# Kernel optimization log

Hardware: AMD Instinct MI355X
Metric: run time of the kernel (lower is better)

Reference implementation:

```python
import jax, jax.numpy as jnp
import numpy as np

# static sizes
B = 32          # graphs
NPER = 1024     # nodes per graph
N0 = B * NPER
F_IN = 128
H = 4           # heads
DH = 32         # per-head dim (128/4)
HID = H * DH    # 128
E = 524288      # edges (avg degree 16)
K1, K2, K3 = 512, 256, 128  # ceil(0.5*nper) per stage
NC = 10


def gcn_agg(h, src, dst, w, n):
    """GCNConv propagation: sym-normalized aggregation with self-loops.
    h: [n,F] already projected; w: [E] edge weight (0 for filtered edges)."""
    deg = jax.ops.segment_sum(w, dst, num_segments=n) + 1.0  # +1 self-loop
    dinv = jax.lax.rsqrt(deg)
    coef = dinv[src] * dinv[dst] * w                          # [E]
    agg = jax.ops.segment_sum(h[src] * coef[:, None], dst, num_segments=n)
    return agg + h / deg[:, None]  # self-loop term: dinv[i]^2 = 1/deg[i]


def mh_gcn(x, W, b, src, dst, w, n):
    """MAGPoolGCNLayer: per-head GCNConv (32->32), relu, concat heads."""
    h = jnp.einsum('nhd,hde->nhe', x.reshape(n, H, DH), W).reshape(n, HID)
    return jax.nn.relu(gcn_agg(h, src, dst, w, n) + b.reshape(HID))


def att_pool(x, src, dst, w, A, psW, psb, n, k):
    """MultiHeadAtt: standard att, complex score, concat pooling, global weight."""
    sub = x.reshape(n, H, DH)
    att = jnp.einsum('nhd,hd->nh', sub, A)            # per-head Linear(32,1)
    cat = (att[:, :, None] * sub).reshape(n, HID)     # score*sub, concat
    score = (gcn_agg(cat @ psW, src, dst, w, n) + psb)[:, 0]  # GCNConv(HID,1)
    nper = n // B
    _, idx = jax.lax.top_k(score.reshape(B, nper), k)  # per-graph topk
    perm = (idx + jnp.arange(B)[:, None] * nper).reshape(-1)
    xn = x[perm] * jnp.tanh(score[perm])[:, None]      # global att weighting
    # filter_adj: remap kept nodes, mask edges touching dropped nodes
    nmap = jnp.full((n,), -1, jnp.int32).at[perm].set(jnp.arange(B * k, dtype=jnp.int32))
    ns, nd = nmap[src], nmap[dst]
    wn = w * ((ns >= 0) & (nd >= 0)).astype(w.dtype)
    return xn, jnp.maximum(ns, 0), jnp.maximum(nd, 0), wn


def readout(x):
    # graphs are contiguous with equal node counts -> reshape readout
    xr = x.reshape(B, -1, x.shape[-1])
    return jnp.concatenate([xr.max(1), xr.mean(1)], axis=1)  # [B, 2*HID]


def setup_inputs():
    key = jax.random.key(0)
    ks = jax.random.split(key, 26)
    gid = jnp.repeat(jnp.arange(B, dtype=jnp.int32), E // B)
    src = jax.random.randint(ks[0], (E,), 0, NPER, dtype=jnp.int32) + gid * NPER
    dst = jax.random.randint(ks[1], (E,), 0, NPER, dtype=jnp.int32) + gid * NPER
    x = jax.random.normal(ks[2], (N0, F_IN), jnp.float32)
    s = 0.1
    def rn(k, shp):
        return jax.random.normal(k, shp, jnp.float32) * s
    return {
        'x': x, 'src': src, 'dst': dst,
        'W1': rn(ks[3], (H, DH, DH)), 'b1': rn(ks[4], (H, DH)), 'A1': rn(ks[5], (H, DH)),
        'ps1W': rn(ks[6], (HID, 1)), 'ps1b': rn(ks[7], (1,)),
        'W2': rn(ks[8], (H, DH, DH)), 'b2': rn(ks[9], (H, DH)), 'A2': rn(ks[10], (H, DH)),
        'ps2W': rn(ks[11], (HID, 1)), 'ps2b': rn(ks[12], (1,)),
        'W3': rn(ks[13], (H, DH, DH)), 'b3': rn(ks[14], (H, DH)), 'A3': rn(ks[15], (H, DH)),
        'ps3W': rn(ks[16], (HID, 1)), 'ps3b': rn(ks[17], (1,)),
        'l1W': rn(ks[18], (2 * HID, HID)), 'l1b': rn(ks[19], (HID,)),
        'l2W': rn(ks[20], (HID, HID // 2)), 'l2b': rn(ks[21], (HID // 2,)),
        'l3W': rn(ks[22], (HID // 2, NC)), 'l3b': rn(ks[23], (NC,)),
    }


def reference(x, src, dst, W1, b1, A1, ps1W, ps1b, W2, b2, A2, ps2W, ps2b,
              W3, b3, A3, ps3W, ps3b, l1W, l1b, l2W, l2b, l3W, l3b):
    w = jnp.ones((E,), x.dtype)
    h = mh_gcn(x, W1, b1, src, dst, w, N0)
    h, s1, d1, w1 = att_pool(h, src, dst, w, A1, ps1W, ps1b, N0, K1)
    r1 = readout(h)
    n1 = B * K1
    h = mh_gcn(h, W2, b2, s1, d1, w1, n1)
    h, s2, d2, w2 = att_pool(h, s1, d1, w1, A2, ps2W, ps2b, n1, K2)
    r2 = readout(h)
    n2 = B * K2
    h = mh_gcn(h, W3, b3, s2, d2, w2, n2)
    h, _, _, _ = att_pool(h, s2, d2, w2, A3, ps3W, ps3b, n2, K3)
    r3 = readout(h)
    z = r1 + r2 + r3                      # [B, 2*HID]
    z = jax.nn.relu(z @ l1W + l1b)        # dropout skipped (eval mode)
    z = jax.nn.relu(z @ l2W + l2b)
    return jax.nn.log_softmax(z @ l3W + l3b, axis=-1)
```

## Files before the change

kernel.cpp:

```cpp
#include <hip/hip_runtime.h>
#include <math.h>

#define BGR 32
#define NPER0 1024
#define N0 (BGR * NPER0)
#define FDIM 128
#define EDG 524288
#define EPG (EDG / BGR)
#define EBLK (EDG / 256)
#define K1 512
#define K2 256
#define K3 128
#define N1 (BGR * K1)
#define N2 (BGR * K2)
#define CAP 64
#define RSEC (BGR * FDIM)

__device__ __forceinline__ unsigned enc_f(float v) {
    unsigned u = __float_as_uint(v);
    return (u & 0x80000000u) ? ~u : (u | 0x80000000u);
}
__device__ __forceinline__ float dec_f(unsigned u) {
    return (u & 0x80000000u) ? __uint_as_float(u ^ 0x80000000u) : __uint_as_float(~u);
}

__global__ void bin_kernel(const int* __restrict__ src, const int* __restrict__ dst,
                           int* __restrict__ cnt, int* __restrict__ slot,
                           unsigned* __restrict__ rmax, float* __restrict__ rsum) {
    if (blockIdx.x < BGR) {
        int z = blockIdx.x * 256 + threadIdx.x;
        rmax[z] = 0u;
        rsum[z] = 0.0f;
    }
    const int g = blockIdx.x & 31, chunk = blockIdx.x >> 5;
    int e = g * EPG + chunk * 256 + threadIdx.x;
    int s = src[e];
    int d = dst[e];
    int p = atomicAdd(&cnt[d], 1);
    if (p < CAP) slot[(size_t)d * CAP + p] = s;
}

__global__ void aggw_kernel(const float* __restrict__ xsrc,
                            const int* __restrict__ permIn,
                            const float* __restrict__ multIn,
                            const int* __restrict__ cnt, const int* __restrict__ slot,
                            const float* __restrict__ W, const float* __restrict__ b,
                            const float* __restrict__ A, const float* __restrict__ psW,
                            float* __restrict__ haOut, float* __restrict__ csd,
                            int nper) {
    __shared__ __align__(16) float sW[4096];
    __shared__ __align__(16) float sY[4][128];
    const int t = threadIdx.x;
    const int w = t >> 6, lane = t & 63;
    const int half = lane >> 5, li = lane & 31;
    const int g = blockIdx.x & 31, chunk = blockIdx.x >> 5;
    const int i = g * nper + chunk * 4 + w;
    {
        float4* d4 = (float4*)sW;
        const float4* s4 = (const float4*)W;
        for (int q = t; q < 1024; q += 256) d4[q] = s4[q];
    }
    const int ci = cnt[i];
    const float di = rsqrtf((float)ci + 1.0f);
    const int c = min(ci, CAP);
    const float4* __restrict__ x4 = (const float4*)xsrc;
    float selfco = di * di;
    size_t selfrow = (size_t)i;
    if (permIn) { selfrow = (size_t)permIn[i]; selfco *= multIn[i]; }
    const float sco = half ? 0.0f : selfco;
    float4 sv = x4[selfrow * 32 + li];
    float4 acc;
    acc.x = sv.x * sco; acc.y = sv.y * sco; acc.z = sv.z * sco; acc.w = sv.w * sco;
    int rowi = 0;
    float codv = 0.0f;
    if (lane < c) {
        int idx = slot[(size_t)i * CAP + lane];
        float dv = rsqrtf((float)cnt[idx] + 1.0f);
        if (permIn) { rowi = permIn[idx]; codv = dv * multIn[idx]; }
        else        { rowi = idx;         codv = dv; }
    }
    const int cp = (c + 1) >> 1;
    int p = 0;
    for (; p + 3 < cp; p += 4) {
        int e0 = 2 * p + half;
        int s0 = __shfl(rowi, e0, 64);
        int s1 = __shfl(rowi, e0 + 2, 64);
        int s2 = __shfl(rowi, e0 + 4, 64);
        int s3 = __shfl(rowi, e0 + 6, 64);
        float c0 = __shfl(codv, e0, 64) * di;
        float c1 = __shfl(codv, e0 + 2, 64) * di;
        float c2 = __shfl(codv, e0 + 4, 64) * di;
        float c3 = __shfl(codv, e0 + 6, 64) * di;
        float4 v0 = x4[(size_t)s0 * 32 + li];
        float4 v1 = x4[(size_t)s1 * 32 + li];
        float4 v2 = x4[(size_t)s2 * 32 + li];
        float4 v3 = x4[(size_t)s3 * 32 + li];
        acc.x = fmaf(v0.x, c0, acc.x); acc.y = fmaf(v0.y, c0, acc.y);
        acc.z = fmaf(v0.z, c0, acc.z); acc.w = fmaf(v0.w, c0, acc.w);
        acc.x = fmaf(v1.x, c1, acc.x); acc.y = fmaf(v1.y, c1, acc.y);
        acc.z = fmaf(v1.z, c1, acc.z); acc.w = fmaf(v1.w, c1, acc.w);
        acc.x = fmaf(v2.x, c2, acc.x); acc.y = fmaf(v2.y, c2, acc.y);
        acc.z = fmaf(v2.z, c2, acc.z); acc.w = fmaf(v2.w, c2, acc.w);
        acc.x = fmaf(v3.x, c3, acc.x); acc.y = fmaf(v3.y, c3, acc.y);
        acc.z = fmaf(v3.z, c3, acc.z); acc.w = fmaf(v3.w, c3, acc.w);
    }
    for (; p < cp; p++) {
        int e = 2 * p + half;
        int s = __shfl(rowi, e, 64);
        float co = __shfl(codv, e, 64) * di;
        float4 v = x4[(size_t)s * 32 + li];
        acc.x = fmaf(v.x, co, acc.x); acc.y = fmaf(v.y, co, acc.y);
        acc.z = fmaf(v.z, co, acc.z); acc.w = fmaf(v.w, co, acc.w);
    }
    acc.x += __shfl_xor(acc.x, 32, 64);
    acc.y += __shfl_xor(acc.y, 32, 64);
    acc.z += __shfl_xor(acc.z, 32, 64);
    acc.w += __shfl_xor(acc.w, 32, 64);
    if (half == 0) *(float4*)(&sY[w][li * 4]) = acc;
    __syncthreads();
    const int f0 = 2 * lane;
    const int h = f0 >> 5, e0h = f0 & 31;
    const float* yp = sY[w] + h * 32;
    const float* wrow = sW + h * 1024 + e0h;
    float2 bb = ((const float2*)b)[lane];
    float ax = bb.x, ay = bb.y;
#pragma unroll
    for (int d = 0; d < 32; d++) {
        float yv = yp[d];
        float2 wv = *(const float2*)(wrow + d * 32);
        ax = fmaf(yv, wv.x, ax);
        ay = fmaf(yv, wv.y, ay);
    }
    float2 o;
    o.x = fmaxf(ax, 0.0f);
    o.y = fmaxf(ay, 0.0f);
    ((float2*)haOut)[(size_t)i * 64 + lane] = o;
    float2 Av = ((const float2*)A)[lane];
    float2 Pv = ((const float2*)psW)[lane];
    float a = o.x * Av.x + o.y * Av.y;
    float pp = o.x * Pv.x + o.y * Pv.y;
#pragma unroll
    for (int d = 8; d > 0; d >>= 1) {
        a += __shfl_down(a, d, 16);
        pp += __shfl_down(pp, d, 16);
    }
    float part = a * pp;
    part += __shfl_down(part, 16, 64);
    part += __shfl_down(part, 32, 64);
    if (lane == 0) csd[i] = part * di;
}

__global__ __launch_bounds__(1024) void topk_kernel(
        const float* __restrict__ csd, const int* __restrict__ cnt,
        const int* __restrict__ slot, const float* __restrict__ psb,
        int nper, int k, int* __restrict__ nmap, int* __restrict__ perm,
        float* __restrict__ mult) {
    __shared__ float cs_l[NPER0];
    __shared__ float sc[NPER0];
    __shared__ unsigned ukey[NPER0];
    __shared__ unsigned hist[256];
    __shared__ unsigned wtot[4];
    __shared__ unsigned sel[2];
    __shared__ int ctr[2];
    const int g = blockIdx.x, t = threadIdx.x;
    const int gnb = g * nper;
    if (t < nper) cs_l[t] = csd[gnb + t];
    if (t == 0) { sel[0] = 0u; sel[1] = (unsigned)k; }
    __syncthreads();
    if (t < nper) {
        int ci = cnt[gnb + t];
        int c = min(ci, CAP);
        const int* srow = slot + (size_t)(gnb + t) * CAP;
        float v = 0.0f;
        for (int j = 0; j < c; j++) v += cs_l[srow[j] - gnb];
        float s = rsqrtf((float)ci + 1.0f) * (v + cs_l[t]) + psb[0];
        sc[t] = s;
        ukey[t] = enc_f(s);
    }
    __syncthreads();
    const int w4 = t >> 6, l = t & 63;
    for (int shift = 24; shift >= 0; shift -= 8) {
        if (t < 256) hist[t] = 0u;
        __syncthreads();
        const unsigned prefix = sel[0];
        const unsigned need = sel[1];
        {
            unsigned u = (t < nper) ? ukey[t] : 0u;
            bool inp = (t < nper) &&
                       ((shift == 24) || ((u >> (shift + 8)) == (prefix >> (shift + 8))));
            int dig = inp ? (int)((u >> shift) & 255u) : -1;
            int cv = inp ? 1 : 0;
#pragma unroll
            for (int d = 1; d < 64; d <<= 1) {
                int od = __shfl_xor(dig, d, 64);
                int oc = __shfl_xor(cv, d, 64);
                if (od == dig) cv = ((l & d) == 0) ? (cv + oc) : 0;
            }
            if (dig >= 0 && cv > 0) atomicAdd(&hist[dig], (unsigned)cv);
        }
        __syncthreads();
        unsigned h = 0, s = 0;
        if (t < 256) {
            h = hist[t];
            s = h;
#pragma unroll
            for (int off = 1; off < 64; off <<= 1) {
                unsigned v2 = __shfl_down(s, off, 64);
                if (l + off < 64) s += v2;
            }
            if (l == 0) wtot[w4] = s;
        }
        __syncthreads();
        if (t < 256) {
            unsigned add = 0;
            for (int ww = w4 + 1; ww < 4; ww++) add += wtot[ww];
            const unsigned sfx = s + add;
            const unsigned gtr = sfx - h;
            if (sfx >= need && gtr < need) {
                sel[0] = prefix | ((unsigned)t << shift);
                sel[1] = need - gtr;
            }
        }
        __syncthreads();
    }
    const unsigned T = sel[0];
    const int need2 = (int)sel[1];
    if (t == 0) { ctr[0] = 0; ctr[1] = k - need2; }
    __syncthreads();
    if (t < nper) {
        unsigned u = ukey[t];
        int newid = -1;
        if (u > T) {
            newid = atomicAdd(&ctr[0], 1);
        } else if (u == T) {
            int s2 = atomicAdd(&ctr[1], 1);
            if (s2 < k) newid = s2;
        }
        nmap[gnb + t] = (newid >= 0) ? g * k + newid : -1;
        if (newid >= 0) {
            perm[g * k + newid] = gnb + t;
            mult[g * k + newid] = tanhf(sc[t]);
        }
    }
}

__global__ void comp_pool(const int* __restrict__ cnt_prev,
                          const int* __restrict__ slot_prev,
                          const int* __restrict__ nmap,
                          int* __restrict__ cnt_next, int* __restrict__ slot_next,
                          const float* __restrict__ ha, const int* __restrict__ perm,
                          const float* __restrict__ mult, int ncomp, int kprev,
                          unsigned* __restrict__ rmax, float* __restrict__ rsum) {
    __shared__ float smax[128], ssum[128];
    const int t = threadIdx.x;
    if (blockIdx.x < ncomp) {
        const int w = t >> 6, lane = t & 63;
        const int b = (blockIdx.x & 31) * kprev + (blockIdx.x >> 5) * 4 + w;
        const int old = perm[b];
        const int c = min(cnt_prev[old], CAP);
        int a = -1;
        if (lane < c) a = nmap[slot_prev[(size_t)old * CAP + lane]];
        unsigned long long mk = __ballot(a >= 0);
        if (a >= 0) {
            int pos = __popcll(mk & ((1ull << lane) - 1ull));
            slot_next[(size_t)b * CAP + pos] = a;
        }
        if (lane == 0) cnt_next[b] = __popcll(mk);
        return;
    }
    const int pb = blockIdx.x - ncomp;
    const int g = pb & 31;
    const int c = pb >> 5;
    const int f = t & 127, half = t >> 7;
    const int base = g * kprev + c * 8;
    float vmax = -1e30f, vsum = 0.0f;
#pragma unroll
    for (int j0 = 0; j0 < 4; j0++) {
        int newid = base + half + j0 * 2;
        int old = perm[newid];
        float m = mult[newid];
        float v = ha[(size_t)old * FDIM + f] * m;
        vmax = fmaxf(vmax, v);
        vsum += v;
    }
    if (half) { smax[f] = vmax; ssum[f] = vsum; }
    __syncthreads();
    if (!half) {
        vmax = fmaxf(vmax, smax[f]);
        vsum += ssum[f];
        atomicMax(&rmax[g * FDIM + f], enc_f(vmax));
        atomicAdd(&rsum[g * FDIM + f], vsum);
    }
}

__global__ __launch_bounds__(1024) void pool3_mlp(
        const float* __restrict__ ha, const int* __restrict__ perm,
        const float* __restrict__ mult,
        const unsigned* __restrict__ rmax, const float* __restrict__ rsum,
        const float* __restrict__ l1W, const float* __restrict__ l1b,
        const float* __restrict__ l2W, const float* __restrict__ l2b,
        const float* __restrict__ l3W, const float* __restrict__ l3b,
        float* __restrict__ out) {
    __shared__ float pm[8][FDIM], ps[8][FDIM];
    __shared__ float sz[256], s1[128], s2[64], s3[16], red[2];
    const int g = blockIdx.x, t = threadIdx.x;
    const int f = t & 127, ch = t >> 7;
    float vmax = -1e30f, vsum = 0.0f;
#pragma unroll
    for (int j = 0; j < K3 / 8; j++) {
        int nid = g * K3 + ch + j * 8;
        int old = perm[nid];
        float m = mult[nid];
        float v = ha[(size_t)old * FDIM + f] * m;
        vmax = fmaxf(vmax, v);
        vsum += v;
    }
    pm[ch][f] = vmax;
    ps[ch][f] = vsum;
    __syncthreads();
    if (t < 128) {
        float M = pm[0][t];
#pragma unroll
        for (int c2 = 1; c2 < 8; c2++) M = fmaxf(M, pm[c2][t]);
        sz[t] = dec_f(rmax[g * FDIM + t]) + dec_f(rmax[RSEC + g * FDIM + t]) + M;
    } else if (t < 256) {
        int f2 = t - 128;
        float S = ps[0][f2];
#pragma unroll
        for (int c2 = 1; c2 < 8; c2++) S += ps[c2][f2];
        sz[t] = rsum[g * FDIM + f2] / (float)K1 + rsum[RSEC + g * FDIM + f2] / (float)K2 +
                S / (float)K3;
    }
    __syncthreads();
    if (t < 128) {
        float acc = l1b[t];
        for (int i = 0; i < 256; i++) acc = fmaf(sz[i], l1W[i * 128 + t], acc);
        s1[t] = fmaxf(acc, 0.0f);
    }
    __syncthreads();
    if (t < 64) {
        float a2 = l2b[t];
        for (int i = 0; i < 128; i++) a2 = fmaf(s1[i], l2W[i * 64 + t], a2);
        s2[t] = fmaxf(a2, 0.0f);
    }
    __syncthreads();
    if (t < 10) {
        float a3 = l3b[t];
        for (int i = 0; i < 64; i++) a3 = fmaf(s2[i], l3W[i * 10 + t], a3);
        s3[t] = a3;
    }
    __syncthreads();
    if (t == 0) {
        float m = -1e30f;
        for (int c = 0; c < 10; c++) m = fmaxf(m, s3[c]);
        float sum = 0.0f;
        for (int c = 0; c < 10; c++) sum += expf(s3[c] - m);
        red[0] = m;
        red[1] = logf(sum);
    }
    __syncthreads();
    if (t < 10) out[g * 10 + t] = s3[t] - red[0] - red[1];
}

extern "C" void kernel_launch(void* const* d_in, const int* in_sizes, int n_in,
                              void* d_out, int out_size, void* d_ws, size_t ws_size,
                              hipStream_t stream) {
    const float* x    = (const float*)d_in[0];
    const int* src0   = (const int*)d_in[1];
    const int* dst0   = (const int*)d_in[2];
    const float* W1   = (const float*)d_in[3];
    const float* b1   = (const float*)d_in[4];
    const float* A1   = (const float*)d_in[5];
    const float* ps1W = (const float*)d_in[6];
    const float* ps1b = (const float*)d_in[7];
    const float* W2   = (const float*)d_in[8];
    const float* b2   = (const float*)d_in[9];
    const float* A2   = (const float*)d_in[10];
    const float* ps2W = (const float*)d_in[11];
    const float* ps2b = (const float*)d_in[12];
    const float* W3   = (const float*)d_in[13];
    const float* b3   = (const float*)d_in[14];
    const float* A3   = (const float*)d_in[15];
    const float* ps3W = (const float*)d_in[16];
    const float* ps3b = (const float*)d_in[17];
    const float* l1W  = (const float*)d_in[18];
    const float* l1b  = (const float*)d_in[19];
    const float* l2W  = (const float*)d_in[20];
    const float* l2b  = (const float*)d_in[21];
    const float* l3W  = (const float*)d_in[22];
    const float* l3b  = (const float*)d_in[23];
    float* out = (float*)d_out;

    char* ws = (char*)d_ws;
    size_t o = 0;
    auto alloc = [&](size_t bytes) -> void* {
        void* p = ws + o;
        o += (bytes + 255) & ~(size_t)255;
        return p;
    };
    float*    ha1   = (float*)alloc((size_t)N0 * FDIM * 4);
    float*    ha2   = (float*)alloc((size_t)N1 * FDIM * 4);
    float*    ha3   = (float*)alloc((size_t)N2 * FDIM * 4);
    int*      cntA  = (int*)alloc(N0 * 4);
    int*      cntB  = (int*)alloc(N1 * 4);
    int*      cntC  = (int*)alloc(N2 * 4);
    int*      slotA = (int*)alloc((size_t)N0 * CAP * 4);
    int*      slotB = (int*)alloc((size_t)N1 * CAP * 4);
    int*      slotC = (int*)alloc((size_t)N2 * CAP * 4);
    float*    cs    = (float*)alloc(N0 * 4);
    int*      nmapA = (int*)alloc(N0 * 4);
    int*      nmapB = (int*)alloc(N1 * 4);
    int*      perm  = (int*)alloc(N1 * 4);
    float*    mult  = (float*)alloc(N1 * 4);
    unsigned* rmax  = (unsigned*)alloc(2 * RSEC * 4);
    float*    rsum  = (float*)alloc(2 * RSEC * 4);

    hipMemsetAsync(cntA, 0, N0 * 4, stream);
    bin_kernel<<<EBLK, 256, 0, stream>>>(src0, dst0, cntA, slotA, rmax, rsum);
    aggw_kernel<<<N0 / 4, 256, 0, stream>>>(x, nullptr, nullptr, cntA, slotA,
                                            W1, b1, A1, ps1W, ha1, cs, NPER0);
    topk_kernel<<<BGR, 1024, 0, stream>>>(cs, cntA, slotA, ps1b, NPER0, K1,
                                          nmapA, perm, mult);

    comp_pool<<<N1 / 4 + BGR * K1 / 8, 256, 0, stream>>>(
        cntA, slotA, nmapA, cntB, slotB, ha1, perm, mult, N1 / 4, K1, rmax, rsum);
    aggw_kernel<<<N1 / 4, 256, 0, stream>>>(ha1, perm, mult, cntB, slotB,
                                            W2, b2, A2, ps2W, ha2, cs, K1);
    topk_kernel<<<BGR, 1024, 0, stream>>>(cs, cntB, slotB, ps2b, K1, K2,
                                          nmapB, perm, mult);

    comp_pool<<<N2 / 4 + BGR * K2 / 8, 256, 0, stream>>>(
        cntB, slotB, nmapB, cntC, slotC, ha2, perm, mult, N2 / 4, K2,
        rmax + RSEC, rsum + RSEC);
    aggw_kernel<<<N2 / 4, 256, 0, stream>>>(ha2, perm, mult, cntC, slotC,
                                            W3, b3, A3, ps3W, ha3, cs, K2);
    topk_kernel<<<BGR, 1024, 0, stream>>>(cs, cntC, slotC, ps3b, K2, K3,
                                          nmapA , perm, mult);

    pool3_mlp<<<BGR, 1024, 0, stream>>>(ha3, perm, mult, rmax, rsum,
                                        l1W, l1b, l2W, l2b, l3W, l3b, out);

    (void)in_sizes; (void)n_in; (void)out_size; (void)ws_size;
}
```

Before: 230.4 us.

## Move readout pooling into aggregation kernel and fuse final topk with MLP

Pooled-feature readout (max/sum atomics) now runs as extra blocks inside the next stage's aggregation kernel instead of alongside edge compaction, leaving compaction as its own lean kernel. The last top-k selection is merged with the stage-3 readout and MLP into one per-graph kernel that keeps perm/mult in shared memory. This drops one launch and the global perm/mult/nmap writes for stage 3. The cost is extra block heterogeneity in the aggregation launch and more shared memory in the fused tail kernel.

```diff
diff --git a/kernel.cpp b/kernel.cpp
--- a/kernel.cpp
+++ b/kernel.cpp
@@ -47,10 +47,39 @@
                             const float* __restrict__ W, const float* __restrict__ b,
                             const float* __restrict__ A, const float* __restrict__ psW,
                             float* __restrict__ haOut, float* __restrict__ csd,
-                            int nper) {
+                            int nper, int naggblk,
+                            unsigned* __restrict__ rmax, float* __restrict__ rsum) {
     __shared__ __align__(16) float sW[4096];
     __shared__ __align__(16) float sY[4][128];
     const int t = threadIdx.x;
+    if (blockIdx.x >= naggblk) {
+        float* smax = sW;
+        float* ssum = sW + 128;
+        const int pb = blockIdx.x - naggblk;
+        const int g = pb & 31;
+        const int c = pb >> 5;
+        const int f = t & 127, hf = t >> 7;
+        const int base = g * nper + c * 8;
+        float vmax = -1e30f, vsum = 0.0f;
+#pragma unroll
+        for (int j0 = 0; j0 < 4; j0++) {
+            int newid = base + hf + j0 * 2;
+            int old = permIn[newid];
+            float m = multIn[newid];
+            float v = xsrc[(size_t)old * FDIM + f] * m;
+            vmax = fmaxf(vmax, v);
+            vsum += v;
+        }
+        if (hf) { smax[f] = vmax; ssum[f] = vsum; }
+        __syncthreads();
+        if (!hf) {
+            vmax = fmaxf(vmax, smax[f]);
+            vsum += ssum[f];
+            atomicMax(&rmax[g * FDIM + f], enc_f(vmax));
+            atomicAdd(&rsum[g * FDIM + f], vsum);
+        }
+        return;
+    }
     const int w = t >> 6, lane = t & 63;
     const int half = lane >> 5, li = lane & 31;
     const int g = blockIdx.x & 31, chunk = blockIdx.x >> 5;
@@ -150,6 +179,27 @@
     if (lane == 0) csd[i] = part * di;
 }
 
+__global__ void comp_kernel(const int* __restrict__ cnt_prev,
+                            const int* __restrict__ slot_prev,
+                            const int* __restrict__ nmap,
+                            const int* __restrict__ perm,
+                            int* __restrict__ cnt_next, int* __restrict__ slot_next,
+                            int knext) {
+    const int t = threadIdx.x;
+    const int w = t >> 6, lane = t & 63;
+    const int b = (blockIdx.x & 31) * knext + (blockIdx.x >> 5) * 4 + w;
+    const int old = perm[b];
+    const int c = min(cnt_prev[old], CAP);
+    int a = -1;
+    if (lane < c) a = nmap[slot_prev[(size_t)old * CAP + lane]];
+    unsigned long long mk = __ballot(a >= 0);
+    if (a >= 0) {
+        int pos = __popcll(mk & ((1ull << lane) - 1ull));
+        slot_next[(size_t)b * CAP + pos] = a;
+    }
+    if (lane == 0) cnt_next[b] = __popcll(mk);
+}
+
 __global__ __launch_bounds__(1024) void topk_kernel(
         const float* __restrict__ csd, const int* __restrict__ cnt,
         const int* __restrict__ slot, const float* __restrict__ psb,
@@ -244,79 +294,121 @@
     }
 }
 
-__global__ void comp_pool(const int* __restrict__ cnt_prev,
-                          const int* __restrict__ slot_prev,
-                          const int* __restrict__ nmap,
-                          int* __restrict__ cnt_next, int* __restrict__ slot_next,
-                          const float* __restrict__ ha, const int* __restrict__ perm,
-                          const float* __restrict__ mult, int ncomp, int kprev,
-                          unsigned* __restrict__ rmax, float* __restrict__ rsum) {
-    __shared__ float smax[128], ssum[128];
-    const int t = threadIdx.x;
-    if (blockIdx.x < ncomp) {
-        const int w = t >> 6, lane = t & 63;
-        const int b = (blockIdx.x & 31) * kprev + (blockIdx.x >> 5) * 4 + w;
-        const int old = perm[b];
-        const int c = min(cnt_prev[old], CAP);
-        int a = -1;
-        if (lane < c) a = nmap[slot_prev[(size_t)old * CAP + lane]];
-        unsigned long long mk = __ballot(a >= 0);
-        if (a >= 0) {
-            int pos = __popcll(mk & ((1ull << lane) - 1ull));
-            slot_next[(size_t)b * CAP + pos] = a;
-        }
-        if (lane == 0) cnt_next[b] = __popcll(mk);
-        return;
-    }
-    const int pb = blockIdx.x - ncomp;
-    const int g = pb & 31;
-    const int c = pb >> 5;
-    const int f = t & 127, half = t >> 7;
-    const int base = g * kprev + c * 8;
-    float vmax = -1e30f, vsum = 0.0f;
-#pragma unroll
-    for (int j0 = 0; j0 < 4; j0++) {
-        int newid = base + half + j0 * 2;
-        int old = perm[newid];
-        float m = mult[newid];
-        float v = ha[(size_t)old * FDIM + f] * m;
-        vmax = fmaxf(vmax, v);
-        vsum += v;
-    }
-    if (half) { smax[f] = vmax; ssum[f] = vsum; }
-    __syncthreads();
-    if (!half) {
-        vmax = fmaxf(vmax, smax[f]);
-        vsum += ssum[f];
-        atomicMax(&rmax[g * FDIM + f], enc_f(vmax));
-        atomicAdd(&rsum[g * FDIM + f], vsum);
-    }
-}
-
-__global__ __launch_bounds__(1024) void pool3_mlp(
-        const float* __restrict__ ha, const int* __restrict__ perm,
-        const float* __restrict__ mult,
+__global__ __launch_bounds__(1024) void topk3_mlp(
+        const float* __restrict__ csd, const int* __restrict__ cnt,
+        const int* __restrict__ slot, const float* __restrict__ psb,
+        const float* __restrict__ ha,
         const unsigned* __restrict__ rmax, const float* __restrict__ rsum,
         const float* __restrict__ l1W, const float* __restrict__ l1b,
         const float* __restrict__ l2W, const float* __restrict__ l2b,
         const float* __restrict__ l3W, const float* __restrict__ l3b,
         float* __restrict__ out) {
+    __shared__ float cs_l[K2];
+    __shared__ float sc[K2];
+    __shared__ unsigned ukey[K2];
+    __shared__ unsigned hist[256];
+    __shared__ unsigned wtot[4];
+    __shared__ unsigned sel[2];
+    __shared__ int ctr[2];
+    __shared__ int perm_l[K3];
+    __shared__ float mult_l[K3];
     __shared__ float pm[8][FDIM], ps[8][FDIM];
     __shared__ float sz[256], s1[128], s2[64], s3[16], red[2];
     const int g = blockIdx.x, t = threadIdx.x;
-    const int f = t & 127, ch = t >> 7;
-    float vmax = -1e30f, vsum = 0.0f;
-#pragma unroll
-    for (int j = 0; j < K3 / 8; j++) {
-        int nid = g * K3 + ch + j * 8;
-        int old = perm[nid];
-        float m = mult[nid];
-        float v = ha[(size_t)old * FDIM + f] * m;
-        vmax = fmaxf(vmax, v);
-        vsum += v;
-    }
-    pm[ch][f] = vmax;
-    ps[ch][f] = vsum;
+    const int gnb = g * K2;
+    if (t < K2) cs_l[t] = csd[gnb + t];
+    if (t == 0) { sel[0] = 0u; sel[1] = (unsigned)K3; }
+    __syncthreads();
+    if (t < K2) {
+        int ci = cnt[gnb + t];
+        int c = min(ci, CAP);
+        const int* srow = slot + (size_t)(gnb + t) * CAP;
+        float v = 0.0f;
+        for (int j = 0; j < c; j++) v += cs_l[srow[j] - gnb];
+        float s = rsqrtf((float)ci + 1.0f) * (v + cs_l[t]) + psb[0];
+        sc[t] = s;
+        ukey[t] = enc_f(s);
+    }
+    __syncthreads();
+    const int w4 = t >> 6, l = t & 63;
+    for (int shift = 24; shift >= 0; shift -= 8) {
+        if (t < 256) hist[t] = 0u;
+        __syncthreads();
+        const unsigned prefix = sel[0];
+        const unsigned need = sel[1];
+        {
+            unsigned u = (t < K2) ? ukey[t] : 0u;
+            bool inp = (t < K2) &&
+                       ((shift == 24) || ((u >> (shift + 8)) == (prefix >> (shift + 8))));
+            int dig = inp ? (int)((u >> shift) & 255u) : -1;
+            int cv = inp ? 1 : 0;
+#pragma unroll
+            for (int d = 1; d < 64; d <<= 1) {
+                int od = __shfl_xor(dig, d, 64);
+                int oc = __shfl_xor(cv, d, 64);
+                if (od == dig) cv = ((l & d) == 0) ? (cv + oc) : 0;
+            }
+            if (dig >= 0 && cv > 0) atomicAdd(&hist[dig], (unsigned)cv);
+        }
+        __syncthreads();
+        unsigned h = 0, s = 0;
+        if (t < 256) {
+            h = hist[t];
+            s = h;
+#pragma unroll
+            for (int off = 1; off < 64; off <<= 1) {
+                unsigned v2 = __shfl_down(s, off, 64);
+                if (l + off < 64) s += v2;
+            }
+            if (l == 0) wtot[w4] = s;
+        }
+        __syncthreads();
+        if (t < 256) {
+            unsigned add = 0;
+            for (int ww = w4 + 1; ww < 4; ww++) add += wtot[ww];
+            const unsigned sfx = s + add;
+            const unsigned gtr = sfx - h;
+            if (sfx >= need && gtr < need) {
+                sel[0] = prefix | ((unsigned)t << shift);
+                sel[1] = need - gtr;
+            }
+        }
+        __syncthreads();
+    }
+    const unsigned T = sel[0];
+    const int need2 = (int)sel[1];
+    if (t == 0) { ctr[0] = 0; ctr[1] = K3 - need2; }
+    __syncthreads();
+    if (t < K2) {
+        unsigned u = ukey[t];
+        int newid = -1;
+        if (u > T) {
+            newid = atomicAdd(&ctr[0], 1);
+        } else if (u == T) {
+            int s2 = atomicAdd(&ctr[1], 1);
+            if (s2 < K3) newid = s2;
+        }
+        if (newid >= 0) {
+            perm_l[newid] = gnb + t;
+            mult_l[newid] = tanhf(sc[t]);
+        }
+    }
+    __syncthreads();
+    {
+        const int f = t & 127, ch = t >> 7;
+        float vmax = -1e30f, vsum = 0.0f;
+#pragma unroll
+        for (int j = 0; j < K3 / 8; j++) {
+            int lid = ch + j * 8;
+            int old = perm_l[lid];
+            float m = mult_l[lid];
+            float v = ha[(size_t)old * FDIM + f] * m;
+            vmax = fmaxf(vmax, v);
+            vsum += v;
+        }
+        pm[ch][f] = vmax;
+        ps[ch][f] = vsum;
+    }
     __syncthreads();
     if (t < 128) {
         float M = pm[0][t];
@@ -418,26 +510,24 @@
     hipMemsetAsync(cntA, 0, N0 * 4, stream);
     bin_kernel<<<EBLK, 256, 0, stream>>>(src0, dst0, cntA, slotA, rmax, rsum);
     aggw_kernel<<<N0 / 4, 256, 0, stream>>>(x, nullptr, nullptr, cntA, slotA,
-                                            W1, b1, A1, ps1W, ha1, cs, NPER0);
+                                            W1, b1, A1, ps1W, ha1, cs, NPER0,
+                                            N0 / 4, nullptr, nullptr);
     topk_kernel<<<BGR, 1024, 0, stream>>>(cs, cntA, slotA, ps1b, NPER0, K1,
                                           nmapA, perm, mult);
 
-    comp_pool<<<N1 / 4 + BGR * K1 / 8, 256, 0, stream>>>(
-        cntA, slotA, nmapA, cntB, slotB, ha1, perm, mult, N1 / 4, K1, rmax, rsum);
-    aggw_kernel<<<N1 / 4, 256, 0, stream>>>(ha1, perm, mult, cntB, slotB,
-                                            W2, b2, A2, ps2W, ha2, cs, K1);
+    comp_kernel<<<N1 / 4, 256, 0, stream>>>(cntA, slotA, nmapA, perm, cntB, slotB, K1);
+    aggw_kernel<<<N1 / 4 + BGR * K1 / 8, 256, 0, stream>>>(
+        ha1, perm, mult, cntB, slotB, W2, b2, A2, ps2W, ha2, cs, K1,
+        N1 / 4, rmax, rsum);
     topk_kernel<<<BGR, 1024, 0, stream>>>(cs, cntB, slotB, ps2b, K1, K2,
                                           nmapB, perm, mult);
 
-    comp_pool<<<N2 / 4 + BGR * K2 / 8, 256, 0, stream>>>(
-        cntB, slotB, nmapB, cntC, slotC, ha2, perm, mult, N2 / 4, K2,
-        rmax + RSEC, rsum + RSEC);
-    aggw_kernel<<<N2 / 4, 256, 0, stream>>>(ha2, perm, mult, cntC, slotC,
-                                            W3, b3, A3, ps3W, ha3, cs, K2);
-    topk_kernel<<<BGR, 1024, 0, stream>>>(cs, cntC, slotC, ps3b, K2, K3,
-                                          nmapA , perm, mult);
-
-    pool3_mlp<<<BGR, 1024, 0, stream>>>(ha3, perm, mult, rmax, rsum,
+    comp_kernel<<<N2 / 4, 256, 0, stream>>>(cntB, slotB, nmapB, perm, cntC, slotC, K2);
+    aggw_kernel<<<N2 / 4 + BGR * K2 / 8, 256, 0, stream>>>(
+        ha2, perm, mult, cntC, slotC, W3, b3, A3, ps3W, ha3, cs, K2,
+        N2 / 4, rmax + RSEC, rsum + RSEC);
+
+    topk3_mlp<<<BGR, 1024, 0, stream>>>(cs, cntC, slotC, ps3b, ha3, rmax, rsum,
                                         l1W, l1b, l2W, l2b, l3W, l3b, out);
 
     (void)in_sizes; (void)n_in; (void)out_size; (void)ws_size;
```

After: 225.8 us. -2.0%, faster.
